# Optimization experiments

Measured on AMD Instinct MI355X. Metric: run time of the kernel, lower is better.

## Reference

```python
import jax, jax.numpy as jnp
import numpy as np
import math

B, S, H, NH = 2, 2048, 1024, 16
HD = H // NH


def setup_inputs() -> dict:
    key = jax.random.key(0)
    k1, k2, k3 = jax.random.split(key, 3)
    hidden_states = jax.random.normal(k1, (B, S, H), dtype=jnp.float32)
    attention_mask = jnp.zeros((B, 1, 1, S), dtype=jnp.float32)
    w_qkv = jax.random.normal(k2, (3 * H, H), dtype=jnp.float32) * (1.0 / math.sqrt(H))
    w_out = jax.random.normal(k3, (H, H), dtype=jnp.float32) * (1.0 / math.sqrt(H))
    gate = jnp.ones((NH,), dtype=jnp.float32)
    return {"hidden_states": hidden_states, "attention_mask": attention_mask,
            "w_qkv": w_qkv, "w_out": w_out, "gate": gate}


def reference(hidden_states, attention_mask, w_qkv, w_out, gate):
    b, s, h = hidden_states.shape
    nh, hd = NH, HD
    # fused QKV projection (no bias)
    qkv = hidden_states @ w_qkv.T                      # [b, s, 3h]
    qkv = qkv.reshape(b, s, 3, nh, hd)
    q, k, v = jnp.moveaxis(qkv, 2, 0)                  # each [b, s, nh, hd]
    q = q.transpose(0, 2, 1, 3)                        # [b, nh, s, hd]
    k = k.transpose(0, 2, 1, 3)
    v = v.transpose(0, 2, 1, 3)
    scores = jnp.einsum('bhqd,bhkd->bhqk', q, k) / math.sqrt(hd)
    scores = scores + attention_mask                   # broadcast [b,1,1,s]
    probs = jax.nn.softmax(scores, axis=-1)            # dropout p=0 -> identity
    ctx = jnp.einsum('bhqk,bhkd->bhqd', probs, v)      # [b, nh, s, hd]
    ctx = ctx.transpose(0, 2, 1, 3)                    # [b, s, nh, hd]
    ctx = ctx * gate[None, None, :, None]              # per-head gating
    ctx = ctx.reshape(b, s, h)
    out = ctx @ w_out.T
    # all gates active (> 1e-4) -> active_gates/num_heads == 1, no rescale
    return out
```

## Files before the change

kernel.cpp:

```cpp
#include <hip/hip_runtime.h>
#include <stdint.h>


typedef __attribute__((ext_vector_type(8))) short short8;
typedef __attribute__((ext_vector_type(4))) float floatx4;
typedef __attribute__((ext_vector_type(4))) unsigned int uint4v;
typedef __attribute__((ext_vector_type(2))) unsigned int uint2v;

__device__ __forceinline__ unsigned short f2bf(float f) {
    unsigned int u = __float_as_uint(f);
    unsigned int r = u + 0x7fffu + ((u >> 16) & 1u);
    return (unsigned short)(r >> 16);
}
#if __has_builtin(__builtin_amdgcn_cvt_pk_bf16_f32)
__device__ __forceinline__ unsigned int pack_bf2(float lo, float hi) {
    auto v = __builtin_amdgcn_cvt_pk_bf16_f32(lo, hi);
    return __builtin_bit_cast(unsigned int, v);
}
#else
__device__ __forceinline__ unsigned int pack_bf2(float lo, float hi) {
    unsigned int a = __float_as_uint(lo) + 0x8000u;
    unsigned int b = __float_as_uint(hi) + 0x8000u;
    return __builtin_amdgcn_perm(b, a, 0x07060302u);
}
#endif

#if __has_builtin(__builtin_amdgcn_exp2f)
#define EXP2(x) __builtin_amdgcn_exp2f(x)
#else
#define EXP2(x) exp2f(x)
#endif

__device__ __forceinline__ void gl2lds16(const void* g, void* l) {
    __builtin_amdgcn_global_load_lds(
        (const __attribute__((address_space(1))) unsigned int*)g,
        (__attribute__((address_space(3))) unsigned int*)l, 16, 0, 0);
}

#define MFMA32(a, b, c) __builtin_amdgcn_mfma_f32_16x16x32_bf16((a), (b), (c), 0, 0, 0)

__global__ __launch_bounds__(256)
void cvt_all(const float* __restrict__ a, const float* __restrict__ b,
             const float* __restrict__ c, const float* __restrict__ mask,
             unsigned short* __restrict__ oa, unsigned short* __restrict__ ob,
             unsigned short* __restrict__ oc, float* __restrict__ m2b)
{
    int i = blockIdx.x * 256 + threadIdx.x;
    if (i >= 2097152) {
        int off = i - 2097152;
        float4 v = *(const float4*)(mask + (size_t)off * 4);
        const float L2E = 1.44269504f, C2 = -14.4269504f;
        float4 w;
        w.x = fmaf(v.x, L2E, C2); w.y = fmaf(v.y, L2E, C2);
        w.z = fmaf(v.z, L2E, C2); w.w = fmaf(v.w, L2E, C2);
        *(float4*)(m2b + (size_t)off * 4) = w;
        return;
    }
    const float* src; unsigned short* dst; int off;
    if (i < 1048576)      { src = a; dst = oa; off = i; }
    else if (i < 1835008) { src = b; dst = ob; off = i - 1048576; }
    else                  { src = c; dst = oc; off = i - 1835008; }
    float4 v = *(const float4*)(src + (size_t)off * 4);
    uint2v w;
    w[0] = pack_bf2(v.x, v.y);
    w[1] = pack_bf2(v.z, v.w);
    *(uint2v*)(dst + (size_t)off * 4) = w;
}

template<int MODE, int BN>
__global__ __launch_bounds__(256)
void gemm_nt(const unsigned short* __restrict__ A,
             const unsigned short* __restrict__ Bm,
             unsigned short* __restrict__ out0,
             unsigned short* __restrict__ out1,
             unsigned short* __restrict__ out2,
             float* __restrict__ outf,
             int N)
{
    __shared__ unsigned char smem[16384 + BN * 128];
    const int K = 1024;
    const int BSL = BN / 32;
    const int tid  = threadIdx.x;
    const int wave = tid >> 6, lane = tid & 63;
    const int l15  = lane & 15, quad = lane >> 4;
    const int wm = wave >> 1, wn = wave & 1;

    int Lid = blockIdx.y * gridDim.x + blockIdx.x;
    int bm = (Lid & 7) * 4 + ((Lid >> 3) & 3);
    int bn = Lid >> 5;

    floatx4 acc[4][BSL];
#pragma unroll
    for (int i = 0; i < 4; i++)
#pragma unroll
        for (int j = 0; j < BSL; j++)
            acc[i][j] = floatx4{0.f, 0.f, 0.f, 0.f};

    int soffA[4], soffB[BSL];
#pragma unroll
    for (int l = 0; l < 4; l++) {
        int s = (wave * 4 + l) * 64 + lane;
        int row = s >> 3;
        soffA[l] = row * K + (((s & 7) ^ (row & 7)) * 8);
    }
#pragma unroll
    for (int l = 0; l < BSL; l++) {
        int s = (wave * BSL + l) * 64 + lane;
        int row = s >> 3;
        soffB[l] = row * K + (((s & 7) ^ (row & 7)) * 8);
    }

    const unsigned short* Abase = A  + (size_t)(bm * 128) * K;
    const unsigned short* Bbase = Bm + (size_t)(bn * BN) * K;

    for (int k0 = 0; k0 < K; k0 += 64) {
        __syncthreads();
#pragma unroll
        for (int l = 0; l < 4; l++)
            gl2lds16(Abase + (size_t)soffA[l] + k0, &smem[(wave * 4 + l) * 1024]);
#pragma unroll
        for (int l = 0; l < BSL; l++)
            gl2lds16(Bbase + (size_t)soffB[l] + k0, &smem[16384 + (wave * BSL + l) * 1024]);
        __syncthreads();
#pragma unroll
        for (int s2 = 0; s2 < 2; s2++) {
            short8 af[4], bfr[BSL];
            int c = s2 * 4 + quad;
#pragma unroll
            for (int i = 0; i < 4; i++) {
                int row = wm * 64 + i * 16 + l15;
                af[i] = *(const short8*)(&smem[row * 128 + ((c ^ (row & 7)) * 16)]);
            }
#pragma unroll
            for (int j = 0; j < BSL; j++) {
                int row = wn * (BN / 2) + j * 16 + l15;
                bfr[j] = *(const short8*)(&smem[16384 + row * 128 + ((c ^ (row & 7)) * 16)]);
            }
#pragma unroll
            for (int i = 0; i < 4; i++)
#pragma unroll
                for (int j = 0; j < BSL; j++)
                    acc[i][j] = MFMA32(af[i], bfr[j], acc[i][j]);
        }
    }

#pragma unroll
    for (int i = 0; i < 4; i++) {
#pragma unroll
        for (int j = 0; j < BSL; j++) {
            int n = bn * BN + wn * (BN / 2) + j * 16 + l15;
#pragma unroll
            for (int r = 0; r < 4; r++) {
                int m = bm * 128 + wm * 64 + i * 16 + quad * 4 + r;
                float fv = acc[i][j][r];
                if (MODE == 1) {
                    outf[(size_t)m * N + n] = fv;
                } else {
                    int t = n >> 10;
                    int h = (n >> 6) & 15;
                    int d = n & 63;
                    int b = m >> 11, si = m & 2047;
                    if (t == 2) {
                        int sip = (si & ~31) | (((si >> 2) & 3) << 3)
                                | (((si >> 4) & 1) << 2) | (si & 3);
                        out2[(((size_t)(b * 16 + h)) * 64 + d) * 2048 + sip] = f2bf(fv);
                    } else {
                        if (t == 0) fv *= 0.18033688f;
                        size_t off = (((size_t)(b * 16 + h)) * 2048 + si) * 64 + d;
                        unsigned short* dst = (t == 0) ? out0 : out1;
                        dst[off] = f2bf(fv);
                    }
                }
            }
        }
    }
}

__global__ __launch_bounds__(256, 2)
void attn_kernel(const unsigned short* __restrict__ Qb,
                 const unsigned short* __restrict__ Kb,
                 const unsigned short* __restrict__ VbT,
                 const float* __restrict__ m2b,
                 const float* __restrict__ gateb,
                 unsigned short* __restrict__ ctx)
{
    __shared__ unsigned char smem[65536];
    const int S = 2048;
    const int tid  = threadIdx.x;
    const int wave = tid >> 6, lane = tid & 63;
    const int l15  = lane & 15, quad = lane >> 4;

    int Lid = blockIdx.y * gridDim.x + blockIdx.x;
    int bh = (Lid & 7) * 4 + ((Lid >> 3) & 3);
    int qc = Lid >> 5;
    const int b = bh >> 4, h = bh & 15;
    const int q0 = qc * 64;

    const size_t headoff = (size_t)bh * S * 64;
    const unsigned short* Qh  = Qb  + headoff;
    const unsigned short* Kh  = Kb  + headoff;
    const unsigned short* VhT = VbT + headoff;
    const float* m2p = m2b + (size_t)b * S;

    const int WB = wave * 16384;

    short8 aq[4][2];
#pragma unroll
    for (int sub = 0; sub < 4; sub++)
#pragma unroll
        for (int s2 = 0; s2 < 2; s2++)
            aq[sub][s2] = *(const short8*)(Qh + (size_t)(q0 + sub * 16 + l15) * 64 + s2 * 32 + quad * 8);

    floatx4 o[4][4];
    floatx4 lq[4];
#pragma unroll
    for (int sub = 0; sub < 4; sub++) {
        lq[sub] = floatx4{0.f, 0.f, 0.f, 0.f};
#pragma unroll
        for (int dt = 0; dt < 4; dt++) o[sub][dt] = floatx4{0.f, 0.f, 0.f, 0.f};
    }

    int koff[4], voff[4];
#pragma unroll
    for (int l = 0; l < 4; l++) {
        int s = l * 64 + lane;
        int key = s >> 3;
        koff[l] = key * 64 + (((s & 7) ^ (key & 7)) * 8);
        int d = s >> 2;
        voff[l] = d * 2048 + (((s & 3) ^ (d & 3)) * 8);
    }
    int qkoff[2];
#pragma unroll
    for (int s2 = 0; s2 < 2; s2++)
        qkoff[s2] = l15 * 128 + (((s2 * 4 + quad) ^ (l15 & 7)) * 16);
    const int pvoff = 4096 + l15 * 64 + ((quad ^ (l15 & 3)) * 16);

    const uint4v onesu = {0x3F803F80u, 0x3F803F80u, 0x3F803F80u, 0x3F803F80u};
    const short8 ONES = __builtin_bit_cast(short8, onesu);

    {
        const unsigned short* kg = Kh + (size_t)(wave * 32) * 64;
        const unsigned short* vg = VhT + wave * 32;
#pragma unroll
        for (int l = 0; l < 4; l++) {
            gl2lds16(kg + koff[l], &smem[WB + l * 1024]);
            gl2lds16(vg + voff[l], &smem[WB + 4096 + l * 1024]);
        }
    }

    for (int i = 0; i < 16; i++) {
        const int kb = (wave + 4 * i) * 32;
        floatx4 mf[2];
#pragma unroll
        for (int t = 0; t < 2; t++)
            mf[t] = *(const floatx4*)(m2p + kb + t * 16 + quad * 4);
        asm volatile("" ::: "memory");
        {
            const int kbn = (wave + 4 * ((i + 1) & 15)) * 32;
            const int hb = WB + ((i + 1) & 1) * 8192;
            const unsigned short* kg = Kh + (size_t)kbn * 64;
            const unsigned short* vg = VhT + kbn;
#pragma unroll
            for (int l = 0; l < 4; l++) {
                gl2lds16(kg + koff[l], &smem[hb + l * 1024]);
                gl2lds16(vg + voff[l], &smem[hb + 4096 + l * 1024]);
            }
        }
        asm volatile("s_waitcnt vmcnt(8)" ::: "memory");

        const int cb = WB + (i & 1) * 8192;
        short8 vf[4];
#pragma unroll
        for (int dt = 0; dt < 4; dt++)
            vf[dt] = *(const short8*)(&smem[cb + pvoff + dt * 1024]);
        short8 kf[2][2];
#pragma unroll
        for (int t = 0; t < 2; t++)
#pragma unroll
            for (int s2 = 0; s2 < 2; s2++)
                kf[t][s2] = *(const short8*)(&smem[cb + qkoff[s2] + t * 2048]);

#pragma unroll
        for (int sub = 0; sub < 4; sub++) {
            floatx4 st0 = MFMA32(kf[0][0], aq[sub][0], mf[0]);
            floatx4 st1 = MFMA32(kf[1][0], aq[sub][0], mf[1]);
            st0 = MFMA32(kf[0][1], aq[sub][1], st0);
            st1 = MFMA32(kf[1][1], aq[sub][1], st1);
            float e00 = EXP2(st0[0]), e01 = EXP2(st0[1]);
            float e02 = EXP2(st0[2]), e03 = EXP2(st0[3]);
            float e10 = EXP2(st1[0]), e11 = EXP2(st1[1]);
            float e12 = EXP2(st1[2]), e13 = EXP2(st1[3]);
            uint4v pu = {pack_bf2(e00, e01), pack_bf2(e02, e03),
                         pack_bf2(e10, e11), pack_bf2(e12, e13)};
            short8 pf = __builtin_bit_cast(short8, pu);
#pragma unroll
            for (int dt = 0; dt < 4; dt++)
                o[sub][dt] = MFMA32(vf[dt], pf, o[sub][dt]);
            lq[sub] = MFMA32(ONES, pf, lq[sub]);
        }
    }

    asm volatile("s_waitcnt vmcnt(0)" ::: "memory");

    floatx4 ro[4];
#pragma unroll
    for (int ph = 0; ph < 2; ph++) {
        __syncthreads();
#pragma unroll
        for (int sub = 0; sub < 4; sub++)
#pragma unroll
            for (int d2 = 0; d2 < 2; d2++)
                *(floatx4*)(&smem[(((wave * 4 + sub) * 2 + d2) * 64 + lane) * 16]) = o[sub][ph * 2 + d2];
        __syncthreads();
#pragma unroll
        for (int d2 = 0; d2 < 2; d2++) {
            floatx4 acc = floatx4{0.f, 0.f, 0.f, 0.f};
#pragma unroll
            for (int w2 = 0; w2 < 4; w2++)
                acc += *(const floatx4*)(&smem[(((w2 * 4 + wave) * 2 + d2) * 64 + lane) * 16]);
            ro[ph * 2 + d2] = acc;
        }
    }
    __syncthreads();
#pragma unroll
    for (int sub = 0; sub < 4; sub++)
        *(floatx4*)(&smem[((wave * 4 + sub) * 64 + lane) * 16]) = lq[sub];
    __syncthreads();
    floatx4 rl = floatx4{0.f, 0.f, 0.f, 0.f};
#pragma unroll
    for (int w2 = 0; w2 < 4; w2++)
        rl += *(const floatx4*)(&smem[((w2 * 4 + wave) * 64 + lane) * 16]);

    float iv = gateb[h] / rl[0];
    size_t base = ((size_t)(b * 2048 + q0 + wave * 16 + l15)) * 1024 + h * 64 + quad * 4;
#pragma unroll
    for (int dt = 0; dt < 4; dt++) {
        uint2v w;
        w[0] = pack_bf2(ro[dt][0] * iv, ro[dt][1] * iv);
        w[1] = pack_bf2(ro[dt][2] * iv, ro[dt][3] * iv);
        *(uint2v*)(ctx + base + dt * 16) = w;
    }
}

extern "C" void kernel_launch(void* const* d_in, const int* in_sizes, int n_in,
                              void* d_out, int out_size, void* d_ws, size_t ws_size,
                              hipStream_t stream)
{
    const float* hidden = (const float*)d_in[0];
    const float* mask   = (const float*)d_in[1];
    const float* w_qkv  = (const float*)d_in[2];
    const float* w_out  = (const float*)d_in[3];
    const float* gate   = (const float*)d_in[4];
    float* out = (float*)d_out;

    unsigned short* q_buf = (unsigned short*)d_ws;
    unsigned short* k_buf = q_buf + 4194304;
    unsigned short* v_buf = k_buf + 4194304;
    unsigned short* c_buf = v_buf + 4194304;
    unsigned short* h_bf  = c_buf + 4194304;
    unsigned short* wq_bf = h_bf  + 4194304;
    unsigned short* wo_bf = wq_bf + 3145728;
    float* m2_buf = (float*)(wo_bf + 1048576);

    cvt_all<<<8196, 256, 0, stream>>>(hidden, w_qkv, w_out, mask,
                                      h_bf, wq_bf, wo_bf, m2_buf);

    gemm_nt<0, 128><<<dim3(24, 32), 256, 0, stream>>>(h_bf, wq_bf, q_buf, k_buf, v_buf, nullptr, 3072);
    attn_kernel<<<dim3(32, 32), 256, 0, stream>>>(q_buf, k_buf, v_buf, m2_buf, gate, c_buf);
    gemm_nt<1, 64><<<dim3(16, 32), 256, 0, stream>>>(c_buf, wo_bf, nullptr, nullptr, nullptr, out, 1024);
}
```

Before: 193.3 us.

## Double-buffer LDS tiles in GEMM to overlap global loads with MFMA

The GEMM mainloop now uses two LDS buffers. It issues the direct-to-LDS loads for the next K step before computing on the current buffer, and uses explicit s_waitcnt vmcnt counts so that only the current tile's loads must finish. This is meant to hide global memory latency behind MFMA work instead of stalling at each barrier. LDS use doubles, which may lower occupancy, and the hardcoded vmcnt values depend on the exact number of outstanding loads per thread.

```diff
diff --git a/kernel.cpp b/kernel.cpp
--- a/kernel.cpp
+++ b/kernel.cpp
@@ -77,8 +77,10 @@
              float* __restrict__ outf,
              int N)
 {
-    __shared__ unsigned char smem[16384 + BN * 128];
+    constexpr int BUF = 16384 + BN * 128;
+    __shared__ unsigned char smem[2 * BUF];
     const int K = 1024;
+    const int NSTEP = 16;
     const int BSL = BN / 32;
     const int tid  = threadIdx.x;
     const int wave = tid >> 6, lane = tid & 63;
@@ -113,15 +115,35 @@
     const unsigned short* Abase = A  + (size_t)(bm * 128) * K;
     const unsigned short* Bbase = Bm + (size_t)(bn * BN) * K;
 
-    for (int k0 = 0; k0 < K; k0 += 64) {
-        __syncthreads();
-#pragma unroll
-        for (int l = 0; l < 4; l++)
-            gl2lds16(Abase + (size_t)soffA[l] + k0, &smem[(wave * 4 + l) * 1024]);
-#pragma unroll
-        for (int l = 0; l < BSL; l++)
-            gl2lds16(Bbase + (size_t)soffB[l] + k0, &smem[16384 + (wave * BSL + l) * 1024]);
-        __syncthreads();
+#pragma unroll
+    for (int l = 0; l < 4; l++)
+        gl2lds16(Abase + (size_t)soffA[l], &smem[(wave * 4 + l) * 1024]);
+#pragma unroll
+    for (int l = 0; l < BSL; l++)
+        gl2lds16(Bbase + (size_t)soffB[l], &smem[16384 + (wave * BSL + l) * 1024]);
+
+    for (int t = 0; t < NSTEP; t++) {
+        const int cb = (t & 1) * BUF;
+        const int nb = ((t + 1) & 1) * BUF;
+        asm volatile("" ::: "memory");
+        __builtin_amdgcn_s_barrier();
+        asm volatile("" ::: "memory");
+        if (t + 1 < NSTEP) {
+            const int k0 = (t + 1) * 64;
+#pragma unroll
+            for (int l = 0; l < 4; l++)
+                gl2lds16(Abase + (size_t)soffA[l] + k0, &smem[nb + (wave * 4 + l) * 1024]);
+#pragma unroll
+            for (int l = 0; l < BSL; l++)
+                gl2lds16(Bbase + (size_t)soffB[l] + k0, &smem[nb + 16384 + (wave * BSL + l) * 1024]);
+            if (BN == 128) asm volatile("s_waitcnt vmcnt(8)" ::: "memory");
+            else           asm volatile("s_waitcnt vmcnt(6)" ::: "memory");
+        } else {
+            asm volatile("s_waitcnt vmcnt(0)" ::: "memory");
+        }
+        __builtin_amdgcn_s_barrier();
+        asm volatile("" ::: "memory");
+
 #pragma unroll
         for (int s2 = 0; s2 < 2; s2++) {
             short8 af[4], bfr[BSL];
@@ -129,12 +151,12 @@
 #pragma unroll
             for (int i = 0; i < 4; i++) {
                 int row = wm * 64 + i * 16 + l15;
-                af[i] = *(const short8*)(&smem[row * 128 + ((c ^ (row & 7)) * 16)]);
+                af[i] = *(const short8*)(&smem[cb + row * 128 + ((c ^ (row & 7)) * 16)]);
             }
 #pragma unroll
             for (int j = 0; j < BSL; j++) {
                 int row = wn * (BN / 2) + j * 16 + l15;
-                bfr[j] = *(const short8*)(&smem[16384 + row * 128 + ((c ^ (row & 7)) * 16)]);
+                bfr[j] = *(const short8*)(&smem[cb + 16384 + row * 128 + ((c ^ (row & 7)) * 16)]);
             }
 #pragma unroll
             for (int i = 0; i < 4; i++)
```

Result: faster. 186.6 us (-3.5%).
